# Optimization experiments

Hardware: AMD Instinct MI355X
Metric: run time of the kernel (lower is better)

Reference implementation:

```python
import jax, jax.numpy as jnp
import numpy as np

N, D, H, C = 50000, 256, 4, 16  # nodes, in_dim, heads, out_channels (hidden_dim)
E = 1600000
NEG_SLOPE = 0.2


def _gatv2_layer(x, src, dst, Wl, bl, Wr, br, att, bias, n_nodes):
    """PyG GATv2Conv (share_weights=False, concat=True, eval mode).
    x: [N, Fin]; Wl/Wr: [Fin, H*C]; att: [H, C]; bias: [H*C].
    """
    xl = (x @ Wl + bl).reshape(n_nodes, H, C)  # source-side transform
    xr = (x @ Wr + br).reshape(n_nodes, H, C)  # target-side transform
    # per-edge attention logits: a^T LeakyReLU(xl_j + xr_i)
    e = jax.nn.leaky_relu(xl[src] + xr[dst], negative_slope=NEG_SLOPE)  # [E,H,C]
    logits = jnp.einsum('ehc,hc->eh', e, att)  # [E,H]
    # scatter-softmax over incoming edges of each target node
    m = jax.ops.segment_max(logits, dst, num_segments=n_nodes)  # [N,H]
    ex = jnp.exp(logits - m[dst])
    denom = jax.ops.segment_sum(ex, dst, num_segments=n_nodes)  # [N,H]
    alpha = ex / denom[dst]  # [E,H]
    out = jax.ops.segment_sum(alpha[:, :, None] * xl[src], dst, num_segments=n_nodes)
    return out.reshape(n_nodes, H * C) + bias


def setup_inputs() -> dict:
    key = jax.random.key(0)
    ks = jax.random.split(key, 16)
    g = lambda k, shp, fan: jax.random.normal(k, shp, jnp.float32) * (1.0 / np.sqrt(fan))
    inp = {
        'x': jax.random.normal(ks[0], (N, D), jnp.float32),
        'edge_index': jax.random.randint(ks[1], (2, E), 0, N, dtype=jnp.int64),
        # conv1: in D -> H*C
        'Wl1': g(ks[2], (D, H * C), D), 'bl1': jnp.zeros((H * C,), jnp.float32),
        'Wr1': g(ks[3], (D, H * C), D), 'br1': jnp.zeros((H * C,), jnp.float32),
        'att1': g(ks[4], (H, C), C), 'bias1': jnp.zeros((H * C,), jnp.float32),
        # conv2: in H*C -> H*C
        'Wl2': g(ks[5], (H * C, H * C), H * C), 'bl2': jnp.zeros((H * C,), jnp.float32),
        'Wr2': g(ks[6], (H * C, H * C), H * C), 'br2': jnp.zeros((H * C,), jnp.float32),
        'att2': g(ks[7], (H, C), C), 'bias2': jnp.zeros((H * C,), jnp.float32),
        # output head: H*C -> D
        'Wo': g(ks[8], (H * C, D), H * C), 'bo': jnp.zeros((D,), jnp.float32),
    }
    return inp


def reference(x, edge_index, Wl1, bl1, Wr1, br1, att1, bias1,
              Wl2, bl2, Wr2, br2, att2, bias2, Wo, bo):
    src, dst = edge_index[0], edge_index[1]
    h = jax.nn.relu(_gatv2_layer(x, src, dst, Wl1, bl1, Wr1, br1, att1, bias1, N))
    h = jax.nn.relu(_gatv2_layer(h, src, dst, Wl2, bl2, Wr2, br2, att2, bias2, N))
    return jax.nn.sigmoid(h @ Wo + bo)  # min_max is None -> no affine rescale
```

## Files before the change

kernel.cpp:

```cpp
#include <hip/hip_runtime.h>
#include <math.h>

#define NN 50000
#define DIN 256
#define HC 64
#define NEG 0.2f
#define TM 64
#define NB 196
#define EPB 4096
#define CAP 36864

typedef short bf16x8 __attribute__((ext_vector_type(8)));
typedef unsigned short ush8 __attribute__((ext_vector_type(8)));
typedef float f32x4 __attribute__((ext_vector_type(4)));

__device__ __forceinline__ unsigned short f2bf(float x) {
    unsigned u = __float_as_uint(x);
    u += 0x7FFFu + ((u >> 16) & 1u);
    return (unsigned short)(u >> 16);
}
__device__ __forceinline__ float bf2f(unsigned short h) {
    return __uint_as_float((unsigned)h << 16);
}

template <int CTRL>
__device__ __forceinline__ float dpp_mov(float x) {
    int r = __builtin_amdgcn_update_dpp(0, __float_as_int(x), CTRL, 0xF, 0xF, true);
    return __int_as_float(r);
}


__global__ __launch_bounds__(256) void bhist_k(const int* __restrict__ dst,
                                               int* __restrict__ bcnt, int E) {
    __shared__ int h[NB];
    int t = threadIdx.x;
    for (int i = t; i < NB; i += 256) h[i] = 0;
    __syncthreads();
    int base = blockIdx.x * 2048 + t;
#pragma unroll
    for (int k = 0; k < 8; ++k) {
        int e = base + k * 256;
        if (e < E) atomicAdd(&h[dst[e] >> 8], 1);
    }
    __syncthreads();
    for (int i = t; i < NB; i += 256)
        if (h[i]) atomicAdd(&bcnt[i], h[i]);
}

__global__ __launch_bounds__(256) void bscan_k(const int* __restrict__ bcnt,
                                               int* __restrict__ boffs,
                                               int* __restrict__ bcursor,
                                               int* __restrict__ offs, int E) {
    __shared__ int s[256];
    int t = threadIdx.x;
    s[t] = (t < NB) ? bcnt[t] : 0;
    __syncthreads();
    for (int off = 1; off < 256; off <<= 1) {
        int v = s[t];
        int u = (t >= off) ? s[t - off] : 0;
        __syncthreads();
        s[t] = v + u;
        __syncthreads();
    }
    if (t < NB) {
        int ex = (t == 0) ? 0 : s[t - 1];
        boffs[t] = ex;
        bcursor[t] = ex;
    }
    if (t == NB) boffs[NB] = s[NB - 1];
    if (t == 0) offs[NN] = E;
}

__global__ __launch_bounds__(1024) void bin_k(const int* __restrict__ src,
                                              const int* __restrict__ dst,
                                              int* __restrict__ bcursor,
                                              unsigned* __restrict__ epair, int E) {
    __shared__ int hist[NB];
    __shared__ int lofs[NB];
    __shared__ int gshift[NB];
    __shared__ int scanb[256];
    __shared__ unsigned pbuf[EPB];
    __shared__ unsigned char abkt[EPB];
    int t = threadIdx.x;
    for (int i = t; i < NB; i += 1024) hist[i] = 0;
    __syncthreads();
    int e0 = blockIdx.x * EPB;
    unsigned p[4]; int bk[4], rk[4]; bool val[4];
#pragma unroll
    for (int k = 0; k < 4; ++k) {
        int e = e0 + k * 1024 + t;
        val[k] = e < E;
        if (val[k]) {
            int s = src[e], d = dst[e];
            p[k] = ((unsigned)s << 8) | (unsigned)(d & 255);
            bk[k] = d >> 8;
            rk[k] = atomicAdd(&hist[bk[k]], 1);
        }
    }
    __syncthreads();
    if (t < 256) scanb[t] = (t < NB) ? hist[t] : 0;
    __syncthreads();
    for (int off = 1; off < 256; off <<= 1) {
        int v = 0, u = 0;
        if (t < 256) { v = scanb[t]; if (t >= off) u = scanb[t - off]; }
        __syncthreads();
        if (t < 256) scanb[t] = v + u;
        __syncthreads();
    }
    if (t < NB) {
        int ex = (t == 0) ? 0 : scanb[t - 1];
        lofs[t] = ex;
        int gb = atomicAdd(&bcursor[t], hist[t]);
        gshift[t] = gb - ex;
    }
    __syncthreads();
    int total = scanb[NB - 1];
#pragma unroll
    for (int k = 0; k < 4; ++k) {
        if (val[k]) {
            int pos = lofs[bk[k]] + rk[k];
            pbuf[pos] = p[k];
            abkt[pos] = (unsigned char)bk[k];
        }
    }
    __syncthreads();
    for (int i = t; i < total; i += 1024) {
        int b = abkt[i];
        epair[gshift[b] + i] = pbuf[i];
    }
}

__global__ __launch_bounds__(1024) void bsort_k(const unsigned* __restrict__ epair,
                                                const int* __restrict__ boffs,
                                                int* __restrict__ offs,
                                                unsigned* __restrict__ ssrc, int n) {
    __shared__ int lhist[256];
    __shared__ int lcur[256];
    __shared__ int scanb[256];
    __shared__ unsigned sbuf[CAP];
    int b = blockIdx.x, t = threadIdx.x;
    int start = boffs[b], end = boffs[b + 1];
    int cnt = end - start;
    if (t < 256) lhist[t] = 0;
    __syncthreads();
    for (int i = t; i < cnt; i += 1024) {
        unsigned p = epair[start + i];
        atomicAdd(&lhist[p & 255], 1);
    }
    __syncthreads();
    if (t < 256) scanb[t] = lhist[t];
    __syncthreads();
    for (int off = 1; off < 256; off <<= 1) {
        int v = 0, u = 0;
        if (t < 256) { v = scanb[t]; if (t >= off) u = scanb[t - off]; }
        __syncthreads();
        if (t < 256) scanb[t] = v + u;
        __syncthreads();
    }
    if (t < 256) {
        int ex = (t == 0) ? 0 : scanb[t - 1];
        lcur[t] = ex;
        int node = b * 256 + t;
        if (node < n) offs[node] = start + ex;
    }
    __syncthreads();
    if (cnt <= CAP) {
        for (int i = t; i < cnt; i += 1024) {
            unsigned p = epair[start + i];
            int r = atomicAdd(&lcur[p & 255], 1);
            sbuf[r] = p & ~255u;
        }
        __syncthreads();
        for (int i = t; i < cnt; i += 1024) ssrc[start + i] = sbuf[i] >> 1;
    } else {
        for (int i = t; i < cnt; i += 1024) {
            unsigned p = epair[start + i];
            int r = atomicAdd(&lcur[p & 255], 1);
            ssrc[start + r] = (p & ~255u) >> 1;
        }
    }
}

__global__ __launch_bounds__(256) void wprep_dual_k(const float* __restrict__ Wl,
                                                    const float* __restrict__ Wr,
                                                    unsigned short* __restrict__ img,
                                                    int K) {
    int i = blockIdx.x * 256 + threadIdx.x;
    int total = (K >> 5) * 10240;
    if (i >= total) return;
    int kk = i % 40;
    int c  = (i / 40) & 127;
    int p  = (i / 5120) & 1;
    int s  = i / 10240;
    unsigned short v = 0;
    if (kk < 32) {
        int k = s * 32 + kk;
        float w = (c < 64) ? Wl[k * HC + c] : Wr[k * HC + (c - 64)];
        unsigned short hi = f2bf(w);
        v = p ? f2bf(w - bf2f(hi)) : hi;
    }
    img[i] = v;
}

__global__ __launch_bounds__(256) void wprep_head_k(const float* __restrict__ Wo,
                                                    unsigned short* __restrict__ img) {
    int i = blockIdx.x * 256 + threadIdx.x;
    if (i >= 40960) return;
    int kk = i % 40;
    int c  = (i / 40) & 127;
    int p  = (i / 5120) & 1;
    int s  = (i / 10240) & 1;
    int h  = i / 20480;
    unsigned short v = 0;
    if (kk < 32) {
        int k = s * 32 + kk;
        float w = Wo[k * DIN + h * 128 + c];
        unsigned short hi = f2bf(w);
        v = p ? f2bf(w - bf2f(hi)) : hi;
    }
    img[i] = v;
}

__global__ __launch_bounds__(256) void gemm_dual_mfma_k(
        const float* __restrict__ A,
        const unsigned short* __restrict__ img,
        const float* __restrict__ bl, const float* __restrict__ br,
        _Float16* __restrict__ xlh, _Float16* __restrict__ xrh,
        int n, int K) {
    __shared__ __attribute__((aligned(16))) unsigned short As[2][64][40];
    __shared__ __attribute__((aligned(16))) unsigned short Bs[2][128][40];
    int t = threadIdx.x;
    int l = t & 63, w = t >> 6;
    int wr = w >> 1, wc = w & 1;
    int lan = l & 15;
    int kb  = (l >> 4) * 8;
    int row0 = blockIdx.x * 64;
    int srow = t >> 2;
    int skq  = (t & 3) * 8;
    bool rok = (row0 + srow) < n;
    const float* aptr = A + (size_t)(row0 + srow) * K + skq;

    f32x4 acc0[4] = {}, acc1[4] = {};

    int nks = K >> 5;
    for (int ks = 0; ks < nks; ++ks) {
        __syncthreads();
        {
            const ush8* src = (const ush8*)(img + (size_t)ks * 10240);
            ush8* dst = (ush8*)&Bs[0][0][0];
            int base = w * 5 * 64 + l;
#pragma unroll
            for (int c2 = 0; c2 < 5; ++c2) {
                int u = base + c2 * 64;
                dst[u] = src[u];
            }
        }
        {
            float4 f0 = make_float4(0.f, 0.f, 0.f, 0.f), f1 = f0;
            if (rok) {
                f0 = *(const float4*)(aptr + ks * 32);
                f1 = *(const float4*)(aptr + ks * 32 + 4);
            }
            float xs[8] = {f0.x, f0.y, f0.z, f0.w, f1.x, f1.y, f1.z, f1.w};
            ush8 hi8, lo8;
#pragma unroll
            for (int j = 0; j < 8; ++j) {
                unsigned short h = f2bf(xs[j]);
                hi8[j] = h;
                lo8[j] = f2bf(xs[j] - bf2f(h));
            }
            *(ush8*)&As[0][srow][skq] = hi8;
            *(ush8*)&As[1][srow][skq] = lo8;
        }
        __syncthreads();
        bf16x8 ah0 = *(const bf16x8*)&As[0][wr * 32 + lan][kb];
        bf16x8 ah1 = *(const bf16x8*)&As[0][wr * 32 + 16 + lan][kb];
        bf16x8 al0 = *(const bf16x8*)&As[1][wr * 32 + lan][kb];
        bf16x8 al1 = *(const bf16x8*)&As[1][wr * 32 + 16 + lan][kb];
#pragma unroll
        for (int cf = 0; cf < 4; ++cf) {
            int bc = wc * 64 + cf * 16 + lan;
            bf16x8 bhv = *(const bf16x8*)&Bs[0][bc][kb];
            bf16x8 blv = *(const bf16x8*)&Bs[1][bc][kb];
            acc0[cf] = __builtin_amdgcn_mfma_f32_16x16x32_bf16(ah0, bhv, acc0[cf], 0, 0, 0);
            acc1[cf] = __builtin_amdgcn_mfma_f32_16x16x32_bf16(ah1, bhv, acc1[cf], 0, 0, 0);
            acc0[cf] = __builtin_amdgcn_mfma_f32_16x16x32_bf16(al0, bhv, acc0[cf], 0, 0, 0);
            acc1[cf] = __builtin_amdgcn_mfma_f32_16x16x32_bf16(al1, bhv, acc1[cf], 0, 0, 0);
            acc0[cf] = __builtin_amdgcn_mfma_f32_16x16x32_bf16(ah0, blv, acc0[cf], 0, 0, 0);
            acc1[cf] = __builtin_amdgcn_mfma_f32_16x16x32_bf16(ah1, blv, acc1[cf], 0, 0, 0);
        }
    }
#pragma unroll
    for (int cf = 0; cf < 4; ++cf) {
        int col = wc * 64 + cf * 16 + lan;
        bool left = col < 64;
        float bv = left ? bl[col] : br[col - 64];
        int c2 = left ? col : col - 64;
        _Float16* dsth = left ? xlh : xrh;
#pragma unroll
        for (int rf = 0; rf < 2; ++rf) {
            f32x4 a = rf ? acc1[cf] : acc0[cf];
            int rbase = row0 + wr * 32 + rf * 16 + (l >> 4) * 4;
#pragma unroll
            for (int r = 0; r < 4; ++r) {
                int grow = rbase + r;
                if (grow < n) dsth[(size_t)grow * HC + c2] = (_Float16)(a[r] + bv);
            }
        }
    }
}

__global__ __launch_bounds__(256) void head_gemm_mfma_k(
        const float* __restrict__ A,
        const unsigned short* __restrict__ img,
        const float* __restrict__ bo,
        float* __restrict__ out, int n) {
    __shared__ __attribute__((aligned(16))) unsigned short As[2][64][40];
    __shared__ __attribute__((aligned(16))) unsigned short Bs[2][128][40];
    int t = threadIdx.x;
    int l = t & 63, w = t >> 6;
    int wr = w >> 1, wc = w & 1;
    int lan = l & 15;
    int kb  = (l >> 4) * 8;
    int row0 = blockIdx.x * 64;
    int coloff = blockIdx.y * 128;
    const unsigned short* himg = img + (size_t)blockIdx.y * 2 * 10240;
    int srow = t >> 2;
    int skq  = (t & 3) * 8;
    bool rok = (row0 + srow) < n;
    const float* aptr = A + (size_t)(row0 + srow) * HC + skq;

    f32x4 acc0[4] = {}, acc1[4] = {};

    for (int ks = 0; ks < 2; ++ks) {
        __syncthreads();
        {
            const ush8* src = (const ush8*)(himg + (size_t)ks * 10240);
            ush8* dst = (ush8*)&Bs[0][0][0];
            int base = w * 5 * 64 + l;
#pragma unroll
            for (int c2 = 0; c2 < 5; ++c2) {
                int u = base + c2 * 64;
                dst[u] = src[u];
            }
        }
        {
            float4 f0 = make_float4(0.f, 0.f, 0.f, 0.f), f1 = f0;
            if (rok) {
                f0 = *(const float4*)(aptr + ks * 32);
                f1 = *(const float4*)(aptr + ks * 32 + 4);
            }
            float xs[8] = {f0.x, f0.y, f0.z, f0.w, f1.x, f1.y, f1.z, f1.w};
            ush8 hi8, lo8;
#pragma unroll
            for (int j = 0; j < 8; ++j) {
                unsigned short h = f2bf(xs[j]);
                hi8[j] = h;
                lo8[j] = f2bf(xs[j] - bf2f(h));
            }
            *(ush8*)&As[0][srow][skq] = hi8;
            *(ush8*)&As[1][srow][skq] = lo8;
        }
        __syncthreads();
        bf16x8 ah0 = *(const bf16x8*)&As[0][wr * 32 + lan][kb];
        bf16x8 ah1 = *(const bf16x8*)&As[0][wr * 32 + 16 + lan][kb];
        bf16x8 al0 = *(const bf16x8*)&As[1][wr * 32 + lan][kb];
        bf16x8 al1 = *(const bf16x8*)&As[1][wr * 32 + 16 + lan][kb];
#pragma unroll
        for (int cf = 0; cf < 4; ++cf) {
            int bc = wc * 64 + cf * 16 + lan;
            bf16x8 bhv = *(const bf16x8*)&Bs[0][bc][kb];
            bf16x8 blv = *(const bf16x8*)&Bs[1][bc][kb];
            acc0[cf] = __builtin_amdgcn_mfma_f32_16x16x32_bf16(ah0, bhv, acc0[cf], 0, 0, 0);
            acc1[cf] = __builtin_amdgcn_mfma_f32_16x16x32_bf16(ah1, bhv, acc1[cf], 0, 0, 0);
            acc0[cf] = __builtin_amdgcn_mfma_f32_16x16x32_bf16(al0, bhv, acc0[cf], 0, 0, 0);
            acc1[cf] = __builtin_amdgcn_mfma_f32_16x16x32_bf16(al1, bhv, acc1[cf], 0, 0, 0);
            acc0[cf] = __builtin_amdgcn_mfma_f32_16x16x32_bf16(ah0, blv, acc0[cf], 0, 0, 0);
            acc1[cf] = __builtin_amdgcn_mfma_f32_16x16x32_bf16(ah1, blv, acc1[cf], 0, 0, 0);
        }
    }
#pragma unroll
    for (int cf = 0; cf < 4; ++cf) {
        int col = coloff + wc * 64 + cf * 16 + lan;
        float bv = bo[col];
#pragma unroll
        for (int rf = 0; rf < 2; ++rf) {
            f32x4 a = rf ? acc1[cf] : acc0[cf];
            int rbase = row0 + wr * 32 + rf * 16 + (l >> 4) * 4;
#pragma unroll
            for (int r = 0; r < 4; ++r) {
                int grow = rbase + r;
                if (grow < n) {
                    float v = a[r] + bv;
                    out[(size_t)grow * DIN + col] = 1.f / (1.f + __expf(-v));
                }
            }
        }
    }
}

union H4 { uint2 u; _Float16 s[4]; };

#define AGRP_BODY(SB, OK)                                                     \
    {                                                                         \
        H4 cv;                                                                \
        cv.u = *(const uint2*)(xhb + (SB) + hoff);                            \
        float xv0 = (float)cv.s[0], xv1 = (float)cv.s[1];                     \
        float xv2 = (float)cv.s[2], xv3 = (float)cv.s[3];                     \
        float s0 = xv0 + xr0, s1 = xv1 + xr1;                                 \
        float s2 = xv2 + xr2, s3 = xv3 + xr3;                                 \
        float tt = at0 * fmaxf(s0, NEG * s0);                                 \
        tt = fmaf(at1, fmaxf(s1, NEG * s1), tt);                              \
        tt = fmaf(at2, fmaxf(s2, NEG * s2), tt);                              \
        tt = fmaf(at3, fmaxf(s3, NEG * s3), tt);                              \
        tt += dpp_mov<0xB1>(tt);                                              \
        tt += dpp_mov<0x4E>(tt);                                              \
        float ex = exp2f(tt);                                                 \
        if (!(OK)) ex = 0.f;                                                  \
        den += ex;                                                            \
        acc0 = fmaf(ex, xv0, acc0); acc1 = fmaf(ex, xv1, acc1);               \
        acc2 = fmaf(ex, xv2, acc2); acc3 = fmaf(ex, xv3, acc3);               \
    }

#define AGRPS(KK)                                                             \
    {                                                                         \
        unsigned sb = (unsigned)__shfl((int)sbv, (KK) * 4 + q);               \
        AGRP_BODY(sb, true)                                                   \
    }

__global__ __launch_bounds__(256) void agg_k(const _Float16* __restrict__ xlh,
                                             const _Float16* __restrict__ xrh,
                                             const float* __restrict__ att,
                                             const float* __restrict__ bias,
                                             const int* __restrict__ offs,
                                             const unsigned* __restrict__ ssb,
                                             float* __restrict__ out, int n) {
    int wave = (blockIdx.x * 256 + threadIdx.x) >> 6;
    int lane = threadIdx.x & 63;
    if (wave >= n) return;
    int q  = lane >> 4;
    int sl = lane & 15;
    const char* xhb = (const char*)xlh;
    unsigned hoff = (unsigned)sl * 8u;
    H4 xq;
    xq.u = *(const uint2*)((const char*)xrh + (size_t)wave * 128 + sl * 8);
    float xr0 = (float)xq.s[0], xr1 = (float)xq.s[1];
    float xr2 = (float)xq.s[2], xr3 = (float)xq.s[3];
    const float LOG2E = 1.44269504088896340736f;
    float4 aq = *(const float4*)(att + sl * 4);
    float at0 = aq.x * LOG2E, at1 = aq.y * LOG2E;
    float at2 = aq.z * LOG2E, at3 = aq.w * LOG2E;
    float acc0 = 0.f, acc1 = 0.f, acc2 = 0.f, acc3 = 0.f;
    float den = 0.f;
    int lo = __builtin_amdgcn_readfirstlane(offs[wave]);
    int hi = __builtin_amdgcn_readfirstlane(offs[wave + 1]);
    int i = lo;
    for (; i + 32 <= hi; i += 32) {
        unsigned sbv = ssb[i + (lane & 31)];
        AGRPS(0) AGRPS(1) AGRPS(2) AGRPS(3)
        AGRPS(4) AGRPS(5) AGRPS(6) AGRPS(7)
    }
    if (i + 16 <= hi) {
        unsigned sbv = ssb[i + (lane & 15)];
        AGRPS(0) AGRPS(1) AGRPS(2) AGRPS(3)
        i += 16;
    }
    for (; i < hi; i += 4) {
        int e = i + q;
        bool ok = e < hi;
        unsigned sb = ssb[ok ? e : (hi - 1)];
        AGRP_BODY(sb, ok)
    }
#pragma unroll
    for (int m = 16; m < 64; m <<= 1) {
        acc0 += __shfl_xor(acc0, m);
        acc1 += __shfl_xor(acc1, m);
        acc2 += __shfl_xor(acc2, m);
        acc3 += __shfl_xor(acc3, m);
        den  += __shfl_xor(den, m);
    }
    if (q == 0) {
        float r = (den > 0.f) ? 1.f / den : 0.f;
        float4 b4 = *(const float4*)(bias + sl * 4);
        float4 o;
        o.x = fmaxf(fmaf(acc0, r, b4.x), 0.f);
        o.y = fmaxf(fmaf(acc1, r, b4.y), 0.f);
        o.z = fmaxf(fmaf(acc2, r, b4.z), 0.f);
        o.w = fmaxf(fmaf(acc3, r, b4.w), 0.f);
        *(float4*)(out + (size_t)wave * HC + sl * 4) = o;
    }
}

extern "C" void kernel_launch(void* const* d_in, const int* in_sizes, int n_in,
                              void* d_out, int out_size, void* d_ws, size_t ws_size,
                              hipStream_t stream) {
    const float* x    = (const float*)d_in[0];
    const int*   ei   = (const int*)d_in[1];
    const float* Wl1  = (const float*)d_in[2];
    const float* bl1  = (const float*)d_in[3];
    const float* Wr1  = (const float*)d_in[4];
    const float* br1  = (const float*)d_in[5];
    const float* att1 = (const float*)d_in[6];
    const float* bias1= (const float*)d_in[7];
    const float* Wl2  = (const float*)d_in[8];
    const float* bl2  = (const float*)d_in[9];
    const float* Wr2  = (const float*)d_in[10];
    const float* br2  = (const float*)d_in[11];
    const float* att2 = (const float*)d_in[12];
    const float* bias2= (const float*)d_in[13];
    const float* Wo   = (const float*)d_in[14];
    const float* bo   = (const float*)d_in[15];
    float* out = (float*)d_out;

    int E = in_sizes[1] / 2;
    const int* srcv = ei;
    const int* dstv = ei + E;

    size_t NF = (size_t)NN * HC;
    float* xl = (float*)d_ws;
    float* xrf = xl + NF;
    float* hb = xrf + NF;
    int* offs        = (int*)(hb + NF);
    unsigned* ssrc   = (unsigned*)(offs + NN + 1);
    int* boffs   = (int*)(ssrc + E);
    int* bcursor = boffs + NB + 1;
    int* bcnt    = bcursor + NB;
    unsigned* epair = (unsigned*)d_out;
    unsigned short* img1 = (unsigned short*)d_out;
    unsigned short* img2 = img1 + 81920;
    unsigned short* imgh = (unsigned short*)xl;
    _Float16* xlh = (_Float16*)((char*)d_out + (16u << 20));
    _Float16* xrh = (_Float16*)xrf;

    hipMemsetAsync(bcnt, 0, NB * sizeof(int), stream);
    bhist_k<<<(E + 2047) / 2048, 256, 0, stream>>>(dstv, bcnt, E);
    bscan_k<<<1, 256, 0, stream>>>(bcnt, boffs, bcursor, offs, E);
    bin_k<<<(E + EPB - 1) / EPB, 1024, 0, stream>>>(srcv, dstv, bcursor, epair, E);
    bsort_k<<<NB, 1024, 0, stream>>>(epair, boffs, offs, ssrc, NN);
    wprep_dual_k<<<320, 256, 0, stream>>>(Wl1, Wr1, img1, DIN);
    wprep_dual_k<<<80, 256, 0, stream>>>(Wl2, Wr2, img2, HC);

    int gb = (NN + TM - 1) / TM;
    gemm_dual_mfma_k<<<gb, 256, 0, stream>>>(x, img1, bl1, br1, xlh, xrh, NN, DIN);
    agg_k<<<(NN + 3) / 4, 256, 0, stream>>>(xlh, xrh, att1, bias1, offs, ssrc, hb, NN);
    gemm_dual_mfma_k<<<gb, 256, 0, stream>>>(hb, img2, bl2, br2, xlh, xrh, NN, HC);
    agg_k<<<(NN + 3) / 4, 256, 0, stream>>>(xlh, xrh, att2, bias2, offs, ssrc, hb, NN);
    wprep_head_k<<<160, 256, 0, stream>>>(Wo, imgh);
    head_gemm_mfma_k<<<dim3(gb, 2), 256, 0, stream>>>(hb, imgh, bo, out, NN);
}
```

Measured before the change: 320.2 us.

## Fuse GEMM, aggregation and head stages into one cooperative persistent kernel

Replaces the six separate launches for weight prep, the two dual GEMMs, the two aggregations and the output head with one cooperative persistent kernel. Phases run as grid-stride loops separated by grid.sync(), and the grid size comes from an occupancy query capped at 2048 blocks. This removes per-launch overhead and the idle tail between kernels. In exchange it adds grid-wide barriers and lower occupancy from the launch-bounds hint, and the persistent loop may balance the irregular aggregation work less well than one wave per node.

```diff
diff --git a/kernel.cpp b/kernel.cpp
--- a/kernel.cpp
+++ b/kernel.cpp
@@ -1,11 +1,13 @@
 #include <hip/hip_runtime.h>
+#include <hip/hip_cooperative_groups.h>
 #include <math.h>
+
+namespace cg = cooperative_groups;
 
 #define NN 50000
 #define DIN 256
 #define HC 64
 #define NEG 0.2f
-#define TM 64
 #define NB 196
 #define EPB 4096
 #define CAP 36864
@@ -181,218 +183,213 @@
     }
 }
 
-__global__ __launch_bounds__(256) void wprep_dual_k(const float* __restrict__ Wl,
-                                                    const float* __restrict__ Wr,
-                                                    unsigned short* __restrict__ img,
-                                                    int K) {
-    int i = blockIdx.x * 256 + threadIdx.x;
+
+__device__ __forceinline__ void wprep_dual_phase(const float* Wl, const float* Wr,
+                                                 unsigned short* img, int K) {
     int total = (K >> 5) * 10240;
-    if (i >= total) return;
-    int kk = i % 40;
-    int c  = (i / 40) & 127;
-    int p  = (i / 5120) & 1;
-    int s  = i / 10240;
-    unsigned short v = 0;
-    if (kk < 32) {
-        int k = s * 32 + kk;
-        float w = (c < 64) ? Wl[k * HC + c] : Wr[k * HC + (c - 64)];
-        unsigned short hi = f2bf(w);
-        v = p ? f2bf(w - bf2f(hi)) : hi;
-    }
-    img[i] = v;
-}
-
-__global__ __launch_bounds__(256) void wprep_head_k(const float* __restrict__ Wo,
-                                                    unsigned short* __restrict__ img) {
-    int i = blockIdx.x * 256 + threadIdx.x;
-    if (i >= 40960) return;
-    int kk = i % 40;
-    int c  = (i / 40) & 127;
-    int p  = (i / 5120) & 1;
-    int s  = (i / 10240) & 1;
-    int h  = i / 20480;
-    unsigned short v = 0;
-    if (kk < 32) {
-        int k = s * 32 + kk;
-        float w = Wo[k * DIN + h * 128 + c];
-        unsigned short hi = f2bf(w);
-        v = p ? f2bf(w - bf2f(hi)) : hi;
-    }
-    img[i] = v;
-}
-
-__global__ __launch_bounds__(256) void gemm_dual_mfma_k(
-        const float* __restrict__ A,
-        const unsigned short* __restrict__ img,
-        const float* __restrict__ bl, const float* __restrict__ br,
-        _Float16* __restrict__ xlh, _Float16* __restrict__ xrh,
-        int n, int K) {
-    __shared__ __attribute__((aligned(16))) unsigned short As[2][64][40];
-    __shared__ __attribute__((aligned(16))) unsigned short Bs[2][128][40];
+    for (int i = blockIdx.x * 256 + threadIdx.x; i < total; i += gridDim.x * 256) {
+        int kk = i % 40;
+        int c  = (i / 40) & 127;
+        int p  = (i / 5120) & 1;
+        int s  = i / 10240;
+        unsigned short v = 0;
+        if (kk < 32) {
+            int k = s * 32 + kk;
+            float w = (c < 64) ? Wl[k * HC + c] : Wr[k * HC + (c - 64)];
+            unsigned short hi = f2bf(w);
+            v = p ? f2bf(w - bf2f(hi)) : hi;
+        }
+        img[i] = v;
+    }
+}
+
+__device__ __forceinline__ void wprep_head_phase(const float* Wo,
+                                                 unsigned short* img) {
+    for (int i = blockIdx.x * 256 + threadIdx.x; i < 40960; i += gridDim.x * 256) {
+        int kk = i % 40;
+        int c  = (i / 40) & 127;
+        int p  = (i / 5120) & 1;
+        int s  = (i / 10240) & 1;
+        int h  = i / 20480;
+        unsigned short v = 0;
+        if (kk < 32) {
+            int k = s * 32 + kk;
+            float w = Wo[k * DIN + h * 128 + c];
+            unsigned short hi = f2bf(w);
+            v = p ? f2bf(w - bf2f(hi)) : hi;
+        }
+        img[i] = v;
+    }
+}
+
+__device__ __forceinline__ void gemm_dual_phase(
+        const float* A, const unsigned short* img,
+        const float* bl, const float* br,
+        _Float16* xlh, _Float16* xrh, int n, int K,
+        unsigned short (&As)[2][64][40], unsigned short (&Bs)[2][128][40]) {
     int t = threadIdx.x;
     int l = t & 63, w = t >> 6;
     int wr = w >> 1, wc = w & 1;
     int lan = l & 15;
     int kb  = (l >> 4) * 8;
-    int row0 = blockIdx.x * 64;
     int srow = t >> 2;
     int skq  = (t & 3) * 8;
-    bool rok = (row0 + srow) < n;
-    const float* aptr = A + (size_t)(row0 + srow) * K + skq;
-
-    f32x4 acc0[4] = {}, acc1[4] = {};
-
+    int nt = (n + 63) >> 6;
     int nks = K >> 5;
-    for (int ks = 0; ks < nks; ++ks) {
-        __syncthreads();
-        {
-            const ush8* src = (const ush8*)(img + (size_t)ks * 10240);
-            ush8* dst = (ush8*)&Bs[0][0][0];
-            int base = w * 5 * 64 + l;
-#pragma unroll
-            for (int c2 = 0; c2 < 5; ++c2) {
-                int u = base + c2 * 64;
-                dst[u] = src[u];
-            }
-        }
-        {
-            float4 f0 = make_float4(0.f, 0.f, 0.f, 0.f), f1 = f0;
-            if (rok) {
-                f0 = *(const float4*)(aptr + ks * 32);
-                f1 = *(const float4*)(aptr + ks * 32 + 4);
-            }
-            float xs[8] = {f0.x, f0.y, f0.z, f0.w, f1.x, f1.y, f1.z, f1.w};
-            ush8 hi8, lo8;
-#pragma unroll
-            for (int j = 0; j < 8; ++j) {
-                unsigned short h = f2bf(xs[j]);
-                hi8[j] = h;
-                lo8[j] = f2bf(xs[j] - bf2f(h));
-            }
-            *(ush8*)&As[0][srow][skq] = hi8;
-            *(ush8*)&As[1][srow][skq] = lo8;
-        }
-        __syncthreads();
-        bf16x8 ah0 = *(const bf16x8*)&As[0][wr * 32 + lan][kb];
-        bf16x8 ah1 = *(const bf16x8*)&As[0][wr * 32 + 16 + lan][kb];
-        bf16x8 al0 = *(const bf16x8*)&As[1][wr * 32 + lan][kb];
-        bf16x8 al1 = *(const bf16x8*)&As[1][wr * 32 + 16 + lan][kb];
+    for (int tile = blockIdx.x; tile < nt; tile += gridDim.x) {
+        int row0 = tile * 64;
+        bool rok = (row0 + srow) < n;
+        const float* aptr = A + (size_t)(row0 + srow) * K + skq;
+        f32x4 acc0[4] = {}, acc1[4] = {};
+        for (int ks = 0; ks < nks; ++ks) {
+            __syncthreads();
+            {
+                const ush8* src = (const ush8*)(img + (size_t)ks * 10240);
+                ush8* dst = (ush8*)&Bs[0][0][0];
+                int base = w * 5 * 64 + l;
+#pragma unroll
+                for (int c2 = 0; c2 < 5; ++c2) {
+                    int u = base + c2 * 64;
+                    dst[u] = src[u];
+                }
+            }
+            {
+                float4 f0 = make_float4(0.f, 0.f, 0.f, 0.f), f1 = f0;
+                if (rok) {
+                    f0 = *(const float4*)(aptr + ks * 32);
+                    f1 = *(const float4*)(aptr + ks * 32 + 4);
+                }
+                float xs[8] = {f0.x, f0.y, f0.z, f0.w, f1.x, f1.y, f1.z, f1.w};
+                ush8 hi8, lo8;
+#pragma unroll
+                for (int j = 0; j < 8; ++j) {
+                    unsigned short h = f2bf(xs[j]);
+                    hi8[j] = h;
+                    lo8[j] = f2bf(xs[j] - bf2f(h));
+                }
+                *(ush8*)&As[0][srow][skq] = hi8;
+                *(ush8*)&As[1][srow][skq] = lo8;
+            }
+            __syncthreads();
+            bf16x8 ah0 = *(const bf16x8*)&As[0][wr * 32 + lan][kb];
+            bf16x8 ah1 = *(const bf16x8*)&As[0][wr * 32 + 16 + lan][kb];
+            bf16x8 al0 = *(const bf16x8*)&As[1][wr * 32 + lan][kb];
+            bf16x8 al1 = *(const bf16x8*)&As[1][wr * 32 + 16 + lan][kb];
+#pragma unroll
+            for (int cf = 0; cf < 4; ++cf) {
+                int bc = wc * 64 + cf * 16 + lan;
+                bf16x8 bhv = *(const bf16x8*)&Bs[0][bc][kb];
+                bf16x8 blv = *(const bf16x8*)&Bs[1][bc][kb];
+                acc0[cf] = __builtin_amdgcn_mfma_f32_16x16x32_bf16(ah0, bhv, acc0[cf], 0, 0, 0);
+                acc1[cf] = __builtin_amdgcn_mfma_f32_16x16x32_bf16(ah1, bhv, acc1[cf], 0, 0, 0);
+                acc0[cf] = __builtin_amdgcn_mfma_f32_16x16x32_bf16(al0, bhv, acc0[cf], 0, 0, 0);
+                acc1[cf] = __builtin_amdgcn_mfma_f32_16x16x32_bf16(al1, bhv, acc1[cf], 0, 0, 0);
+                acc0[cf] = __builtin_amdgcn_mfma_f32_16x16x32_bf16(ah0, blv, acc0[cf], 0, 0, 0);
+                acc1[cf] = __builtin_amdgcn_mfma_f32_16x16x32_bf16(ah1, blv, acc1[cf], 0, 0, 0);
+            }
+        }
 #pragma unroll
         for (int cf = 0; cf < 4; ++cf) {
-            int bc = wc * 64 + cf * 16 + lan;
-            bf16x8 bhv = *(const bf16x8*)&Bs[0][bc][kb];
-            bf16x8 blv = *(const bf16x8*)&Bs[1][bc][kb];
-            acc0[cf] = __builtin_amdgcn_mfma_f32_16x16x32_bf16(ah0, bhv, acc0[cf], 0, 0, 0);
-            acc1[cf] = __builtin_amdgcn_mfma_f32_16x16x32_bf16(ah1, bhv, acc1[cf], 0, 0, 0);
-            acc0[cf] = __builtin_amdgcn_mfma_f32_16x16x32_bf16(al0, bhv, acc0[cf], 0, 0, 0);
-            acc1[cf] = __builtin_amdgcn_mfma_f32_16x16x32_bf16(al1, bhv, acc1[cf], 0, 0, 0);
-            acc0[cf] = __builtin_amdgcn_mfma_f32_16x16x32_bf16(ah0, blv, acc0[cf], 0, 0, 0);
-            acc1[cf] = __builtin_amdgcn_mfma_f32_16x16x32_bf16(ah1, blv, acc1[cf], 0, 0, 0);
-        }
-    }
-#pragma unroll
-    for (int cf = 0; cf < 4; ++cf) {
-        int col = wc * 64 + cf * 16 + lan;
-        bool left = col < 64;
-        float bv = left ? bl[col] : br[col - 64];
-        int c2 = left ? col : col - 64;
-        _Float16* dsth = left ? xlh : xrh;
-#pragma unroll
-        for (int rf = 0; rf < 2; ++rf) {
-            f32x4 a = rf ? acc1[cf] : acc0[cf];
-            int rbase = row0 + wr * 32 + rf * 16 + (l >> 4) * 4;
-#pragma unroll
-            for (int r = 0; r < 4; ++r) {
-                int grow = rbase + r;
-                if (grow < n) dsth[(size_t)grow * HC + c2] = (_Float16)(a[r] + bv);
-            }
-        }
-    }
-}
-
-__global__ __launch_bounds__(256) void head_gemm_mfma_k(
-        const float* __restrict__ A,
-        const unsigned short* __restrict__ img,
-        const float* __restrict__ bo,
-        float* __restrict__ out, int n) {
-    __shared__ __attribute__((aligned(16))) unsigned short As[2][64][40];
-    __shared__ __attribute__((aligned(16))) unsigned short Bs[2][128][40];
+            int col = wc * 64 + cf * 16 + lan;
+            bool left = col < 64;
+            float bv = left ? bl[col] : br[col - 64];
+            int c2 = left ? col : col - 64;
+            _Float16* dsth = left ? xlh : xrh;
+#pragma unroll
+            for (int rf = 0; rf < 2; ++rf) {
+                f32x4 a = rf ? acc1[cf] : acc0[cf];
+                int rbase = row0 + wr * 32 + rf * 16 + (l >> 4) * 4;
+#pragma unroll
+                for (int r = 0; r < 4; ++r) {
+                    int grow = rbase + r;
+                    if (grow < n) dsth[(size_t)grow * HC + c2] = (_Float16)(a[r] + bv);
+                }
+            }
+        }
+    }
+}
+
+__device__ __forceinline__ void head_phase(
+        const float* A, const unsigned short* img, const float* bo,
+        float* outp, int n,
+        unsigned short (&As)[2][64][40], unsigned short (&Bs)[2][128][40]) {
     int t = threadIdx.x;
     int l = t & 63, w = t >> 6;
     int wr = w >> 1, wc = w & 1;
     int lan = l & 15;
     int kb  = (l >> 4) * 8;
-    int row0 = blockIdx.x * 64;
-    int coloff = blockIdx.y * 128;
-    const unsigned short* himg = img + (size_t)blockIdx.y * 2 * 10240;
     int srow = t >> 2;
     int skq  = (t & 3) * 8;
-    bool rok = (row0 + srow) < n;
-    const float* aptr = A + (size_t)(row0 + srow) * HC + skq;
-
-    f32x4 acc0[4] = {}, acc1[4] = {};
-
-    for (int ks = 0; ks < 2; ++ks) {
-        __syncthreads();
-        {
-            const ush8* src = (const ush8*)(himg + (size_t)ks * 10240);
-            ush8* dst = (ush8*)&Bs[0][0][0];
-            int base = w * 5 * 64 + l;
-#pragma unroll
-            for (int c2 = 0; c2 < 5; ++c2) {
-                int u = base + c2 * 64;
-                dst[u] = src[u];
-            }
-        }
-        {
-            float4 f0 = make_float4(0.f, 0.f, 0.f, 0.f), f1 = f0;
-            if (rok) {
-                f0 = *(const float4*)(aptr + ks * 32);
-                f1 = *(const float4*)(aptr + ks * 32 + 4);
-            }
-            float xs[8] = {f0.x, f0.y, f0.z, f0.w, f1.x, f1.y, f1.z, f1.w};
-            ush8 hi8, lo8;
-#pragma unroll
-            for (int j = 0; j < 8; ++j) {
-                unsigned short h = f2bf(xs[j]);
-                hi8[j] = h;
-                lo8[j] = f2bf(xs[j] - bf2f(h));
-            }
-            *(ush8*)&As[0][srow][skq] = hi8;
-            *(ush8*)&As[1][srow][skq] = lo8;
-        }
-        __syncthreads();
-        bf16x8 ah0 = *(const bf16x8*)&As[0][wr * 32 + lan][kb];
-        bf16x8 ah1 = *(const bf16x8*)&As[0][wr * 32 + 16 + lan][kb];
-        bf16x8 al0 = *(const bf16x8*)&As[1][wr * 32 + lan][kb];
-        bf16x8 al1 = *(const bf16x8*)&As[1][wr * 32 + 16 + lan][kb];
+    int nt = ((n + 63) >> 6) * 2;
+    for (int tile = blockIdx.x; tile < nt; tile += gridDim.x) {
+        int row0 = (tile >> 1) * 64;
+        int coloff = (tile & 1) * 128;
+        const unsigned short* himg = img + (size_t)(tile & 1) * 2 * 10240;
+        bool rok = (row0 + srow) < n;
+        const float* aptr = A + (size_t)(row0 + srow) * HC + skq;
+        f32x4 acc0[4] = {}, acc1[4] = {};
+        for (int ks = 0; ks < 2; ++ks) {
+            __syncthreads();
+            {
+                const ush8* src = (const ush8*)(himg + (size_t)ks * 10240);
+                ush8* dst = (ush8*)&Bs[0][0][0];
+                int base = w * 5 * 64 + l;
+#pragma unroll
+                for (int c2 = 0; c2 < 5; ++c2) {
+                    int u = base + c2 * 64;
+                    dst[u] = src[u];
+                }
+            }
+            {
+                float4 f0 = make_float4(0.f, 0.f, 0.f, 0.f), f1 = f0;
+                if (rok) {
+                    f0 = *(const float4*)(aptr + ks * 32);
+                    f1 = *(const float4*)(aptr + ks * 32 + 4);
+                }
+                float xs[8] = {f0.x, f0.y, f0.z, f0.w, f1.x, f1.y, f1.z, f1.w};
+                ush8 hi8, lo8;
+#pragma unroll
+                for (int j = 0; j < 8; ++j) {
+                    unsigned short h = f2bf(xs[j]);
+                    hi8[j] = h;
+                    lo8[j] = f2bf(xs[j] - bf2f(h));
+                }
+                *(ush8*)&As[0][srow][skq] = hi8;
+                *(ush8*)&As[1][srow][skq] = lo8;
+            }
+            __syncthreads();
+            bf16x8 ah0 = *(const bf16x8*)&As[0][wr * 32 + lan][kb];
+            bf16x8 ah1 = *(const bf16x8*)&As[0][wr * 32 + 16 + lan][kb];
+            bf16x8 al0 = *(const bf16x8*)&As[1][wr * 32 + lan][kb];
+            bf16x8 al1 = *(const bf16x8*)&As[1][wr * 32 + 16 + lan][kb];
+#pragma unroll
+            for (int cf = 0; cf < 4; ++cf) {
+                int bc = wc * 64 + cf * 16 + lan;
+                bf16x8 bhv = *(const bf16x8*)&Bs[0][bc][kb];
+                bf16x8 blv = *(const bf16x8*)&Bs[1][bc][kb];
+                acc0[cf] = __builtin_amdgcn_mfma_f32_16x16x32_bf16(ah0, bhv, acc0[cf], 0, 0, 0);
+                acc1[cf] = __builtin_amdgcn_mfma_f32_16x16x32_bf16(ah1, bhv, acc1[cf], 0, 0, 0);
+                acc0[cf] = __builtin_amdgcn_mfma_f32_16x16x32_bf16(al0, bhv, acc0[cf], 0, 0, 0);
+                acc1[cf] = __builtin_amdgcn_mfma_f32_16x16x32_bf16(al1, bhv, acc1[cf], 0, 0, 0);
+                acc0[cf] = __builtin_amdgcn_mfma_f32_16x16x32_bf16(ah0, blv, acc0[cf], 0, 0, 0);
+                acc1[cf] = __builtin_amdgcn_mfma_f32_16x16x32_bf16(ah1, blv, acc1[cf], 0, 0, 0);
+            }
+        }
 #pragma unroll
         for (int cf = 0; cf < 4; ++cf) {
-            int bc = wc * 64 + cf * 16 + lan;
-            bf16x8 bhv = *(const bf16x8*)&Bs[0][bc][kb];
-            bf16x8 blv = *(const bf16x8*)&Bs[1][bc][kb];
-            acc0[cf] = __builtin_amdgcn_mfma_f32_16x16x32_bf16(ah0, bhv, acc0[cf], 0, 0, 0);
-            acc1[cf] = __builtin_amdgcn_mfma_f32_16x16x32_bf16(ah1, bhv, acc1[cf], 0, 0, 0);
-            acc0[cf] = __builtin_amdgcn_mfma_f32_16x16x32_bf16(al0, bhv, acc0[cf], 0, 0, 0);
-            acc1[cf] = __builtin_amdgcn_mfma_f32_16x16x32_bf16(al1, bhv, acc1[cf], 0, 0, 0);
-            acc0[cf] = __builtin_amdgcn_mfma_f32_16x16x32_bf16(ah0, blv, acc0[cf], 0, 0, 0);
-            acc1[cf] = __builtin_amdgcn_mfma_f32_16x16x32_bf16(ah1, blv, acc1[cf], 0, 0, 0);
-        }
-    }
-#pragma unroll
-    for (int cf = 0; cf < 4; ++cf) {
-        int col = coloff + wc * 64 + cf * 16 + lan;
-        float bv = bo[col];
-#pragma unroll
-        for (int rf = 0; rf < 2; ++rf) {
-            f32x4 a = rf ? acc1[cf] : acc0[cf];
-            int rbase = row0 + wr * 32 + rf * 16 + (l >> 4) * 4;
-#pragma unroll
-            for (int r = 0; r < 4; ++r) {
-                int grow = rbase + r;
-                if (grow < n) {
-                    float v = a[r] + bv;
-                    out[(size_t)grow * DIN + col] = 1.f / (1.f + __expf(-v));
+            int col = coloff + wc * 64 + cf * 16 + lan;
+            float bv = bo[col];
+#pragma unroll
+            for (int rf = 0; rf < 2; ++rf) {
+                f32x4 a = rf ? acc1[cf] : acc0[cf];
+                int rbase = row0 + wr * 32 + rf * 16 + (l >> 4) * 4;
+#pragma unroll
+                for (int r = 0; r < 4; ++r) {
+                    int grow = rbase + r;
+                    if (grow < n) {
+                        float v = a[r] + bv;
+                        outp[(size_t)grow * DIN + col] = 1.f / (1.f + __expf(-v));
+                    }
                 }
             }
         }
@@ -428,67 +425,95 @@
         AGRP_BODY(sb, true)                                                   \
     }
 
-__global__ __launch_bounds__(256) void agg_k(const _Float16* __restrict__ xlh,
-                                             const _Float16* __restrict__ xrh,
-                                             const float* __restrict__ att,
-                                             const float* __restrict__ bias,
-                                             const int* __restrict__ offs,
-                                             const unsigned* __restrict__ ssb,
-                                             float* __restrict__ out, int n) {
-    int wave = (blockIdx.x * 256 + threadIdx.x) >> 6;
+__device__ void agg_phase(const _Float16* xlh, const _Float16* xrh,
+                          const float* att, const float* bias,
+                          const int* offs, const unsigned* ssb,
+                          float* outp, int n) {
     int lane = threadIdx.x & 63;
-    if (wave >= n) return;
     int q  = lane >> 4;
     int sl = lane & 15;
     const char* xhb = (const char*)xlh;
     unsigned hoff = (unsigned)sl * 8u;
-    H4 xq;
-    xq.u = *(const uint2*)((const char*)xrh + (size_t)wave * 128 + sl * 8);
-    float xr0 = (float)xq.s[0], xr1 = (float)xq.s[1];
-    float xr2 = (float)xq.s[2], xr3 = (float)xq.s[3];
     const float LOG2E = 1.44269504088896340736f;
     float4 aq = *(const float4*)(att + sl * 4);
     float at0 = aq.x * LOG2E, at1 = aq.y * LOG2E;
     float at2 = aq.z * LOG2E, at3 = aq.w * LOG2E;
-    float acc0 = 0.f, acc1 = 0.f, acc2 = 0.f, acc3 = 0.f;
-    float den = 0.f;
-    int lo = __builtin_amdgcn_readfirstlane(offs[wave]);
-    int hi = __builtin_amdgcn_readfirstlane(offs[wave + 1]);
-    int i = lo;
-    for (; i + 32 <= hi; i += 32) {
-        unsigned sbv = ssb[i + (lane & 31)];
-        AGRPS(0) AGRPS(1) AGRPS(2) AGRPS(3)
-        AGRPS(4) AGRPS(5) AGRPS(6) AGRPS(7)
-    }
-    if (i + 16 <= hi) {
-        unsigned sbv = ssb[i + (lane & 15)];
-        AGRPS(0) AGRPS(1) AGRPS(2) AGRPS(3)
-        i += 16;
-    }
-    for (; i < hi; i += 4) {
-        int e = i + q;
-        bool ok = e < hi;
-        unsigned sb = ssb[ok ? e : (hi - 1)];
-        AGRP_BODY(sb, ok)
-    }
-#pragma unroll
-    for (int m = 16; m < 64; m <<= 1) {
-        acc0 += __shfl_xor(acc0, m);
-        acc1 += __shfl_xor(acc1, m);
-        acc2 += __shfl_xor(acc2, m);
-        acc3 += __shfl_xor(acc3, m);
-        den  += __shfl_xor(den, m);
-    }
-    if (q == 0) {
-        float r = (den > 0.f) ? 1.f / den : 0.f;
-        float4 b4 = *(const float4*)(bias + sl * 4);
-        float4 o;
-        o.x = fmaxf(fmaf(acc0, r, b4.x), 0.f);
-        o.y = fmaxf(fmaf(acc1, r, b4.y), 0.f);
-        o.z = fmaxf(fmaf(acc2, r, b4.z), 0.f);
-        o.w = fmaxf(fmaf(acc3, r, b4.w), 0.f);
-        *(float4*)(out + (size_t)wave * HC + sl * 4) = o;
-    }
+    float4 b4 = *(const float4*)(bias + sl * 4);
+    int wave0 = (blockIdx.x * 256 + threadIdx.x) >> 6;
+    int wstride = (gridDim.x * 256) >> 6;
+    for (int wave = wave0; wave < n; wave += wstride) {
+        H4 xq;
+        xq.u = *(const uint2*)((const char*)xrh + (size_t)wave * 128 + sl * 8);
+        float xr0 = (float)xq.s[0], xr1 = (float)xq.s[1];
+        float xr2 = (float)xq.s[2], xr3 = (float)xq.s[3];
+        float acc0 = 0.f, acc1 = 0.f, acc2 = 0.f, acc3 = 0.f;
+        float den = 0.f;
+        int lo = __builtin_amdgcn_readfirstlane(offs[wave]);
+        int hi = __builtin_amdgcn_readfirstlane(offs[wave + 1]);
+        int i = lo;
+        for (; i + 32 <= hi; i += 32) {
+            unsigned sbv = ssb[i + (lane & 31)];
+            AGRPS(0) AGRPS(1) AGRPS(2) AGRPS(3)
+            AGRPS(4) AGRPS(5) AGRPS(6) AGRPS(7)
+        }
+        if (i + 16 <= hi) {
+            unsigned sbv = ssb[i + (lane & 15)];
+            AGRPS(0) AGRPS(1) AGRPS(2) AGRPS(3)
+            i += 16;
+        }
+        for (; i < hi; i += 4) {
+            int e = i + q;
+            bool ok = e < hi;
+            unsigned sb = ssb[ok ? e : (hi - 1)];
+            AGRP_BODY(sb, ok)
+        }
+#pragma unroll
+        for (int m = 16; m < 64; m <<= 1) {
+            acc0 += __shfl_xor(acc0, m);
+            acc1 += __shfl_xor(acc1, m);
+            acc2 += __shfl_xor(acc2, m);
+            acc3 += __shfl_xor(acc3, m);
+            den  += __shfl_xor(den, m);
+        }
+        if (q == 0) {
+            float r = (den > 0.f) ? 1.f / den : 0.f;
+            float4 o;
+            o.x = fmaxf(fmaf(acc0, r, b4.x), 0.f);
+            o.y = fmaxf(fmaf(acc1, r, b4.y), 0.f);
+            o.z = fmaxf(fmaf(acc2, r, b4.z), 0.f);
+            o.w = fmaxf(fmaf(acc3, r, b4.w), 0.f);
+            *(float4*)(outp + (size_t)wave * HC + sl * 4) = o;
+        }
+    }
+}
+
+__global__ __launch_bounds__(256, 4) void mega_k(
+        const float* x,
+        const float* Wl1, const float* bl1, const float* Wr1, const float* br1,
+        const float* att1, const float* bias1,
+        const float* Wl2, const float* bl2, const float* Wr2, const float* br2,
+        const float* att2, const float* bias2,
+        const float* Wo, const float* bo,
+        unsigned short* img1, unsigned short* img2, unsigned short* imgh,
+        _Float16* xlh, _Float16* xrh, float* hb,
+        const int* offs, const unsigned* ssrc, float* out) {
+    __shared__ __attribute__((aligned(16))) unsigned short As[2][64][40];
+    __shared__ __attribute__((aligned(16))) unsigned short Bs[2][128][40];
+    cg::grid_group grid = cg::this_grid();
+
+    wprep_dual_phase(Wl1, Wr1, img1, DIN);
+    wprep_dual_phase(Wl2, Wr2, img2, HC);
+    wprep_head_phase(Wo, imgh);
+    grid.sync();
+    gemm_dual_phase(x, img1, bl1, br1, xlh, xrh, NN, DIN, As, Bs);
+    grid.sync();
+    agg_phase(xlh, xrh, att1, bias1, offs, ssrc, hb, NN);
+    grid.sync();
+    gemm_dual_phase(hb, img2, bl2, br2, xlh, xrh, NN, HC, As, Bs);
+    grid.sync();
+    agg_phase(xlh, xrh, att2, bias2, offs, ssrc, hb, NN);
+    grid.sync();
+    head_phase(hb, imgh, bo, out, NN, As, Bs);
 }
 
 extern "C" void kernel_launch(void* const* d_in, const int* in_sizes, int n_in,
@@ -537,14 +562,25 @@
     bscan_k<<<1, 256, 0, stream>>>(bcnt, boffs, bcursor, offs, E);
     bin_k<<<(E + EPB - 1) / EPB, 1024, 0, stream>>>(srcv, dstv, bcursor, epair, E);
     bsort_k<<<NB, 1024, 0, stream>>>(epair, boffs, offs, ssrc, NN);
-    wprep_dual_k<<<320, 256, 0, stream>>>(Wl1, Wr1, img1, DIN);
-    wprep_dual_k<<<80, 256, 0, stream>>>(Wl2, Wr2, img2, HC);
-
-    int gb = (NN + TM - 1) / TM;
-    gemm_dual_mfma_k<<<gb, 256, 0, stream>>>(x, img1, bl1, br1, xlh, xrh, NN, DIN);
-    agg_k<<<(NN + 3) / 4, 256, 0, stream>>>(xlh, xrh, att1, bias1, offs, ssrc, hb, NN);
-    gemm_dual_mfma_k<<<gb, 256, 0, stream>>>(hb, img2, bl2, br2, xlh, xrh, NN, HC);
-    agg_k<<<(NN + 3) / 4, 256, 0, stream>>>(xlh, xrh, att2, bias2, offs, ssrc, hb, NN);
-    wprep_head_k<<<160, 256, 0, stream>>>(Wo, imgh);
-    head_gemm_mfma_k<<<dim3(gb, 2), 256, 0, stream>>>(hb, imgh, bo, out, NN);
-}
+
+    static int megaGrid = 0;
+    if (megaGrid == 0) {
+        int mb = 0;
+        hipOccupancyMaxActiveBlocksPerMultiprocessor(&mb, mega_k, 256, 0);
+        if (mb < 1) mb = 1;
+        megaGrid = mb * 256;
+        if (megaGrid > 2048) megaGrid = 2048;
+    }
+    void* args[] = {
+        (void*)&x,
+        (void*)&Wl1, (void*)&bl1, (void*)&Wr1, (void*)&br1,
+        (void*)&att1, (void*)&bias1,
+        (void*)&Wl2, (void*)&bl2, (void*)&Wr2, (void*)&br2,
+        (void*)&att2, (void*)&bias2,
+        (void*)&Wo, (void*)&bo,
+        (void*)&img1, (void*)&img2, (void*)&imgh,
+        (void*)&xlh, (void*)&xrh, (void*)&hb,
+        (void*)&offs, (void*)&ssrc, (void*)&out,
+    };
+    hipLaunchCooperativeKernel(mega_k, dim3(megaGrid), dim3(256), args, 0, stream);
+}
```

New measurement: 760.5 us. +137.5%, slower.
